# Performance work log

Measured on AMD Instinct MI355X. Metric: run time of the kernel, lower is better.

Reference implementation:

```python
import jax, jax.numpy as jnp
import numpy as np

NUM_EMBEDDINGS = 1024
EMBEDDING_DIM = 256

def setup_inputs() -> dict:
    key = jax.random.key(0)
    k1, k2 = jax.random.split(key)
    x = jax.random.normal(k1, (8, 16, 32, 32, EMBEDDING_DIM), dtype=jnp.float32)
    embeddings = jax.random.normal(k2, (NUM_EMBEDDINGS, EMBEDDING_DIM), dtype=jnp.float32)
    return {"x": x, "embeddings": embeddings}

def reference(x, embeddings):
    # Flatten all leading dims to tokens: [N, D]
    flat = x.reshape(-1, EMBEDDING_DIM)
    # Squared euclidean distances via ||a||^2 + ||b||^2 - 2 a.b  -> [N, K]
    sim = jnp.matmul(flat, embeddings.T)
    distances = (jnp.sum(flat * flat, axis=1, keepdims=True)
                 + jnp.sum(embeddings * embeddings, axis=1)
                 - 2.0 * sim)
    encoding_indices = jnp.argmin(distances, axis=1)  # [N]
    quantized = embeddings[encoding_indices].reshape(x.shape)
    # Perplexity from code usage histogram (mean of one-hot == normalized counts)
    counts = jnp.zeros((NUM_EMBEDDINGS,), dtype=jnp.float32).at[encoding_indices].add(1.0)
    avg_probs = counts / flat.shape[0]
    perplexity = jnp.exp(-jnp.sum(avg_probs * jnp.log(avg_probs + 1e-10)))
    return quantized, perplexity
```

## Files before the change

### kernel.cpp

```cpp
#include <hip/hip_runtime.h>
#include <math.h>
#include <stdint.h>

#define NTOK 131072
#define DIM  256
#define KEMB 1024

typedef _Float16 f16x8 __attribute__((ext_vector_type(8)));
typedef float    f32x4 __attribute__((ext_vector_type(4)));

#define FLAG_CAP 65536
#define FLAG_THR 8u

static __device__ __forceinline__ unsigned umin32(unsigned a, unsigned b){ return a<b?a:b; }
static __device__ __forceinline__ unsigned umax32(unsigned a, unsigned b){ return a>b?a:b; }

static __device__ __forceinline__ void gload_lds16(const void* g, void* l) {
    __builtin_amdgcn_global_load_lds(
        (const __attribute__((address_space(1))) unsigned int*)g,
        (__attribute__((address_space(3))) unsigned int*)l, 16, 0, 0);
}

static __device__ __forceinline__ void split_hl(const float4& f0, const float4& f1,
                                                f16x8& h, f16x8& l) {
    float v[8] = {f0.x, f0.y, f0.z, f0.w, f1.x, f1.y, f1.z, f1.w};
    #pragma unroll
    for (int e = 0; e < 8; ++e) {
        const _Float16 hi = (_Float16)v[e];
        h[e] = hi;
        l[e] = (_Float16)(v[e] - (float)hi);
    }
}

__global__ __launch_bounds__(64) void prep_kernel(const float* __restrict__ emb,
                                                  float* __restrict__ eNorm,
                                                  float* __restrict__ cst2,
                                                  unsigned* __restrict__ counts,
                                                  unsigned* __restrict__ flagCnt,
                                                  _Float16* __restrict__ img_hi,
                                                  _Float16* __restrict__ img_lo,
                                                  _Float16* __restrict__ img2) {
    const int k = blockIdx.x;
    const int lane = threadIdx.x;
    const float4 v = *reinterpret_cast<const float4*>(emb + (size_t)k * DIM + lane * 4);
    float s = v.x * v.x + v.y * v.y + v.z * v.z + v.w * v.w;
    #pragma unroll
    for (int m = 32; m; m >>= 1) s += __shfl_xor(s, m, 64);
    if (lane == 0) {
        eNorm[k] = s;
        cst2[k]  = s + 512.0f;
        counts[k] = 0u;
        if (k == 0) *flagCnt = 0u;
    }
    if (lane < 32) {
        const int p = lane;
        const int sl = p ^ (k & 7);
        const float4 s0 = *reinterpret_cast<const float4*>(emb + (size_t)k * DIM + sl * 8);
        const float4 s1 = *reinterpret_cast<const float4*>(emb + (size_t)k * DIM + sl * 8 + 4);
        f16x8 h, l;
        split_hl(s0, s1, h, l);
        *reinterpret_cast<f16x8*>(img_hi + (size_t)k * 256 + p * 8) = h;
        *reinterpret_cast<f16x8*>(img_lo + (size_t)k * 256 + p * 8) = l;
        const int kk = p >> 2, g = p & 3;
        const int ec = k >> 4, c = k & 15;
        const float4 f0 = *reinterpret_cast<const float4*>(emb + (size_t)k * DIM + p * 8);
        const float4 f1 = *reinterpret_cast<const float4*>(emb + (size_t)k * DIM + p * 8 + 4);
        f16x8 h2, l2;
        split_hl(f0, f1, h2, l2);
        *reinterpret_cast<f16x8*>(img2 + (size_t)ec * 4096 + kk * 512 + (g * 16 + c) * 8) = h2;
    }
}

__global__ __launch_bounds__(256, 2) void vq_main(const float* __restrict__ x,
                                                  const float* __restrict__ emb,
                                                  const _Float16* __restrict__ img2,
                                                  const float* __restrict__ cst2,
                                                  int* __restrict__ idxArr,
                                                  unsigned* __restrict__ counts,
                                                  unsigned* __restrict__ flagCnt,
                                                  unsigned* __restrict__ flagList,
                                                  float* __restrict__ out) {
    __shared__ int idx_s[256];

    const int tid  = threadIdx.x;
    const int wv   = tid >> 6;
    const int lane = tid & 63;
    const int g    = lane >> 4;
    const int c    = lane & 15;
    const int T0   = blockIdx.x * 256;
    const int T0w  = T0 + wv * 64;

    f16x8 a[4][8];
    #pragma unroll
    for (int i = 0; i < 4; ++i) {
        const float* xr = x + (size_t)(T0w + i * 16 + c) * DIM + g * 8;
        #pragma unroll
        for (int kk = 0; kk < 8; ++kk) {
            const float4 f0 = *reinterpret_cast<const float4*>(xr + kk * 32);
            const float4 f1 = *reinterpret_cast<const float4*>(xr + kk * 32 + 4);
            a[i][kk] = (f16x8){(_Float16)f0.x, (_Float16)f0.y, (_Float16)f0.z, (_Float16)f0.w,
                               (_Float16)f1.x, (_Float16)f1.y, (_Float16)f1.z, (_Float16)f1.w};
        }
    }

    unsigned m1[16], m2[16];
    #pragma unroll
    for (int t = 0; t < 16; ++t) { m1[t] = 0xFFFFFFFFu; m2[t] = 0xFFFFFFFFu; }

    const _Float16* ibase = img2 + lane * 8;

#define LOADB(DST, CSTD, EC) do {                                              \
        _Pragma("unroll")                                                      \
        for (int _kk = 0; _kk < 8; ++_kk)                                      \
            DST[_kk] = *reinterpret_cast<const f16x8*>(                        \
                ibase + (size_t)(EC) * 4096 + _kk * 512);                      \
        CSTD = cst2[(EC) * 16 + c];                                            \
    } while (0)

#define COMPUTE(BUF, CST, EC) do {                                             \
        f32x4 _acc[4];                                                         \
        _Pragma("unroll")                                                      \
        for (int _i = 0; _i < 4; ++_i) _acc[_i] = (f32x4){0.f, 0.f, 0.f, 0.f}; \
        _Pragma("unroll")                                                      \
        for (int _kk = 0; _kk < 8; ++_kk)                                      \
            _Pragma("unroll")                                                  \
            for (int _i = 0; _i < 4; ++_i)                                     \
                _acc[_i] = __builtin_amdgcn_mfma_f32_16x16x32_f16(             \
                    a[_i][_kk], BUF[_kk], _acc[_i], 0, 0, 0);                  \
        const int _col = (EC) * 16 + c;                                        \
        _Pragma("unroll")                                                      \
        for (int _i = 0; _i < 4; ++_i)                                         \
            _Pragma("unroll")                                                  \
            for (int _e = 0; _e < 4; ++_e) {                                   \
                const float    _d = fmaf(_acc[_i][_e], -2.0f, CST);            \
                const unsigned _k = (__builtin_bit_cast(unsigned, _d)          \
                                     & 0xFFFFFC00u) | (unsigned)_col;          \
                const int _t = _i * 4 + _e;                                    \
                m2[_t] = umin32(m2[_t], umax32(_k, m1[_t]));                   \
                m1[_t] = umin32(m1[_t], _k);                                   \
            }                                                                  \
    } while (0)

    f16x8 bA[8], bB[8];
    float cstA, cstB;
    LOADB(bA, cstA, 0);

    for (int ec2 = 0; ec2 < 32; ++ec2) {
        const int ec0 = ec2 * 2;
        LOADB(bB, cstB, ec0 + 1);
        COMPUTE(bA, cstA, ec0);
        if (ec0 + 2 < 64) LOADB(bA, cstA, ec0 + 2);
        COMPUTE(bB, cstB, ec0 + 1);
    }
#undef LOADB
#undef COMPUTE

    #pragma unroll
    for (int off = 1; off < 16; off <<= 1) {
        #pragma unroll
        for (int t = 0; t < 16; ++t) {
            const unsigned o1 = __shfl_xor(m1[t], off, 64);
            const unsigned o2 = __shfl_xor(m2[t], off, 64);
            const unsigned nm2 = umin32(umin32(m2[t], o2), umax32(m1[t], o1));
            m1[t] = umin32(m1[t], o1);
            m2[t] = nm2;
        }
    }

    if (c == 0) {
        #pragma unroll
        for (int t = 0; t < 16; ++t) {
            const int i   = t >> 2;
            const int e   = t & 3;
            const int row = i * 16 + g * 4 + e;
            const int idx = (int)(m1[t] & 1023u);
            idx_s[wv * 64 + row] = idx;
            idxArr[T0w + row] = idx;
            atomicAdd(&counts[idx], 1u);
            if (((m2[t] >> 10) - (m1[t] >> 10)) < FLAG_THR) {
                const unsigned pos = atomicAdd(flagCnt, 1u);
                if (pos < FLAG_CAP) flagList[pos] = (unsigned)(T0w + row);
            }
        }
    }
    __syncthreads();

    #pragma unroll 4
    for (int s = 0; s < 64; ++s) {
        const int fi  = s * 256 + tid;
        const int row = fi >> 6;
        const int q4  = fi & 63;
        const int em  = idx_s[row];
        *reinterpret_cast<float4*>(out + (size_t)(T0 + row) * DIM + q4 * 4) =
            *reinterpret_cast<const float4*>(emb + (size_t)em * DIM + q4 * 4);
    }
}

__global__ __launch_bounds__(256) void fixup_refine(const float* __restrict__ x,
                                                    const _Float16* __restrict__ img_hi,
                                                    const _Float16* __restrict__ img_lo,
                                                    const float* __restrict__ cst2,
                                                    const unsigned* __restrict__ flagCnt,
                                                    const unsigned* __restrict__ flagList,
                                                    uint2* __restrict__ refTop) {
    __shared__ _Float16 Bh[16384];
    __shared__ _Float16 Bl[16384];
    __shared__ float cst_s[1024];

    const unsigned nf = umin32(*flagCnt, (unsigned)FLAG_CAP);
    if (blockIdx.x * 64u >= nf) return;

    const int tid  = threadIdx.x;
    const int wv   = tid >> 6;
    const int lane = tid & 63;
    const int g    = lane >> 4;
    const int c    = lane & 15;
    const unsigned base = (blockIdx.x * 4u + (unsigned)wv) * 16u;

    *reinterpret_cast<float4*>(&cst_s[tid * 4]) =
        *reinterpret_cast<const float4*>(&cst2[tid * 4]);

    const unsigned myTok = flagList[(base + c) < nf ? (base + c) : 0];
    f16x8 ah[8], al[8];
    {
        const float* xr = x + (size_t)myTok * DIM + g * 8;
        #pragma unroll
        for (int kk = 0; kk < 8; ++kk) {
            const float4 f0 = *reinterpret_cast<const float4*>(xr + kk * 32);
            const float4 f1 = *reinterpret_cast<const float4*>(xr + kk * 32 + 4);
            split_hl(f0, f1, ah[kk], al[kk]);
        }
    }

    unsigned m1[4], m2[4];
    #pragma unroll
    for (int e = 0; e < 4; ++e) { m1[e] = 0xFFFFFFFFu; m2[e] = 0xFFFFFFFFu; }

    for (int ec = 0; ec < 16; ++ec) {
        __syncthreads();
        #pragma unroll
        for (int i = 0; i < 8; ++i) {
            gload_lds16((const char*)img_hi + ec * 32768 + (i * 256 + tid) * 16,
                        (char*)&Bh[0] + i * 4096 + wv * 1024);
            gload_lds16((const char*)img_lo + ec * 32768 + (i * 256 + tid) * 16,
                        (char*)&Bl[0] + i * 4096 + wv * 1024);
        }
        __syncthreads();

        f32x4 acc[4];
        #pragma unroll
        for (int j = 0; j < 4; ++j) acc[j] = (f32x4){0.f, 0.f, 0.f, 0.f};

        #pragma unroll
        for (int kk = 0; kk < 8; ++kk) {
            #pragma unroll
            for (int j = 0; j < 4; ++j) {
                const int row = j * 16 + c;
                const int off = row * 256 + (((kk * 4 + g) ^ (row & 7)) << 3);
                const f16x8 bh = *reinterpret_cast<const f16x8*>(&Bh[off]);
                const f16x8 bl = *reinterpret_cast<const f16x8*>(&Bl[off]);
                acc[j] = __builtin_amdgcn_mfma_f32_16x16x32_f16(ah[kk], bh, acc[j], 0, 0, 0);
                acc[j] = __builtin_amdgcn_mfma_f32_16x16x32_f16(ah[kk], bl, acc[j], 0, 0, 0);
                acc[j] = __builtin_amdgcn_mfma_f32_16x16x32_f16(al[kk], bh, acc[j], 0, 0, 0);
            }
        }

        #pragma unroll
        for (int j = 0; j < 4; ++j) {
            const int   col = ec * 64 + j * 16 + c;
            const float cst = cst_s[col];
            #pragma unroll
            for (int e = 0; e < 4; ++e) {
                const float    d   = fmaf(acc[j][e], -2.0f, cst);
                const unsigned key = (__builtin_bit_cast(unsigned, d) & 0xFFFFFC00u) | (unsigned)col;
                m2[e] = umin32(m2[e], umax32(key, m1[e]));
                m1[e] = umin32(m1[e], key);
            }
        }
    }

    #pragma unroll
    for (int off = 1; off < 16; off <<= 1) {
        #pragma unroll
        for (int e = 0; e < 4; ++e) {
            const unsigned o1 = __shfl_xor(m1[e], off, 64);
            const unsigned o2 = __shfl_xor(m2[e], off, 64);
            const unsigned nm2 = umin32(umin32(m2[e], o2), umax32(m1[e], o1));
            m1[e] = umin32(m1[e], o1);
            m2[e] = nm2;
        }
    }

    if (c == 0) {
        #pragma unroll
        for (int e = 0; e < 4; ++e) {
            const unsigned pos = base + (unsigned)(g * 4 + e);
            if (pos < nf) refTop[pos] = make_uint2(m1[e], m2[e]);
        }
    }
}

__global__ __launch_bounds__(256) void fixup_exact(const float* __restrict__ x,
                                                   const float* __restrict__ emb,
                                                   const float* __restrict__ eNorm,
                                                   const unsigned* __restrict__ flagCnt,
                                                   const unsigned* __restrict__ flagList,
                                                   const uint2* __restrict__ refTop,
                                                   int* __restrict__ idxArr,
                                                   unsigned* __restrict__ counts,
                                                   float* __restrict__ out) {
    const unsigned nf = umin32(*flagCnt, (unsigned)FLAG_CAP);
    const int tid  = threadIdx.x;
    const int wv   = tid >> 6;
    const int lane = tid & 63;

    for (unsigned pos = blockIdx.x * 4u + (unsigned)wv; pos < nf; pos += gridDim.x * 4u) {
        const unsigned tok = flagList[pos];
        const uint2 tk = refTop[pos];
        const int e1 = (int)(tk.x & 1023u);
        const int e2 = (int)(tk.y & 1023u);

        const float4 xv = *reinterpret_cast<const float4*>(x   + (size_t)tok * DIM + lane * 4);
        const float4 v1 = *reinterpret_cast<const float4*>(emb + (size_t)e1  * DIM + lane * 4);
        const float4 v2 = *reinterpret_cast<const float4*>(emb + (size_t)e2  * DIM + lane * 4);
        float p1 = xv.x * v1.x + xv.y * v1.y + xv.z * v1.z + xv.w * v1.w;
        float p2 = xv.x * v2.x + xv.y * v2.y + xv.z * v2.z + xv.w * v2.w;
        #pragma unroll
        for (int off = 1; off < 64; off <<= 1) {
            p1 += __shfl_xor(p1, off, 64);
            p2 += __shfl_xor(p2, off, 64);
        }
        const float d1 = eNorm[e1] - 2.0f * p1;
        const float d2 = eNorm[e2] - 2.0f * p2;
        const bool pick2 = (d2 < d1) || (d2 == d1 && e2 < e1);
        const int  ni   = pick2 ? e2 : e1;
        const int  old  = idxArr[tok];
        if (ni != old) {
            if (lane == 0) {
                idxArr[tok] = ni;
                atomicSub(&counts[old], 1u);
                atomicAdd(&counts[ni], 1u);
            }
            const float4 nv = pick2 ? v2 : v1;
            *reinterpret_cast<float4*>(out + (size_t)tok * DIM + lane * 4) = nv;
        }
    }
}

__global__ __launch_bounds__(256) void perp_kernel(const unsigned* __restrict__ counts,
                                                   float* __restrict__ out_perp) {
    __shared__ float red[256];
    const int tid = threadIdx.x;
    float s = 0.0f;
    for (int i = tid; i < KEMB; i += 256) {
        const float p = (float)counts[i] / (float)NTOK;
        s += p * logf(p + 1e-10f);
    }
    red[tid] = s;
    __syncthreads();
    for (int off = 128; off; off >>= 1) {
        if (tid < off) red[tid] += red[tid + off];
        __syncthreads();
    }
    if (tid == 0) *out_perp = expf(-red[0]);
}

extern "C" void kernel_launch(void* const* d_in, const int* in_sizes, int n_in,
                              void* d_out, int out_size, void* d_ws, size_t ws_size,
                              hipStream_t stream) {
    (void)in_sizes; (void)n_in; (void)out_size; (void)ws_size;
    const float* x   = (const float*)d_in[0];
    const float* emb = (const float*)d_in[1];
    float* out = (float*)d_out;

    char* ws = (char*)d_ws;
    float*     eNorm    = (float*)(ws);
    float*     cst2     = (float*)(ws + 4096);
    unsigned*  counts   = (unsigned*)(ws + 8192);
    unsigned*  flagCnt  = (unsigned*)(ws + 12288);
    unsigned*  flagList = (unsigned*)(ws + 16384);
    int*       idxArr   = (int*)(ws + 278528);
    _Float16*  img_hi   = (_Float16*)(ws + 802816);
    _Float16*  img_lo   = (_Float16*)(ws + 1327104);
    uint2*     refTop   = (uint2*)(ws + 1851392);
    _Float16*  img2     = (_Float16*)(ws + 2363392);

    prep_kernel<<<KEMB, 64, 0, stream>>>(emb, eNorm, cst2, counts, flagCnt,
                                         img_hi, img_lo, img2);
    vq_main<<<NTOK / 256, 256, 0, stream>>>(x, emb, img2, cst2, idxArr, counts,
                                            flagCnt, flagList, out);
    fixup_refine<<<1024, 256, 0, stream>>>(x, img_hi, img_lo, cst2, flagCnt, flagList, refTop);
    fixup_exact<<<2048, 256, 0, stream>>>(x, emb, eNorm, flagCnt, flagList, refTop,
                                          idxArr, counts, out);
    perp_kernel<<<1, 256, 0, stream>>>(counts, out + (size_t)NTOK * DIM);
}
```

Baseline: 207.2 us.

## Software-pipeline MFMA and argmin fold across codebook chunks, stage norms in LDS

Splits the per-chunk work into an MFMA phase and a distance/argmin fold phase, then interleaves them so the fold of one chunk overlaps the MFMAs of the next. This aims to hide the VALU fold latency behind matrix-core work. Codebook norms are also staged once into shared memory, which replaces per-chunk global loads and adds a block barrier. It costs a second set of accumulator registers, which could raise register pressure under the two-waves launch bound.

```diff
diff --git a/kernel.cpp b/kernel.cpp
--- a/kernel.cpp
+++ b/kernel.cpp
@@ -80,6 +80,7 @@
                                                   unsigned* __restrict__ flagCnt,
                                                   unsigned* __restrict__ flagList,
                                                   float* __restrict__ out) {
+    __shared__ float cst_s[1024];
     __shared__ int idx_s[256];
 
     const int tid  = threadIdx.x;
@@ -90,6 +91,9 @@
     const int T0   = blockIdx.x * 256;
     const int T0w  = T0 + wv * 64;
 
+    *reinterpret_cast<float4*>(&cst_s[tid * 4]) =
+        *reinterpret_cast<const float4*>(&cst2[tid * 4]);
+
     f16x8 a[4][8];
     #pragma unroll
     for (int i = 0; i < 4; ++i) {
@@ -109,30 +113,34 @@
 
     const _Float16* ibase = img2 + lane * 8;
 
-#define LOADB(DST, CSTD, EC) do {                                              \
+    __syncthreads();
+
+#define LOADB(DST, EC) do {                                                    \
         _Pragma("unroll")                                                      \
         for (int _kk = 0; _kk < 8; ++_kk)                                      \
             DST[_kk] = *reinterpret_cast<const f16x8*>(                        \
                 ibase + (size_t)(EC) * 4096 + _kk * 512);                      \
-        CSTD = cst2[(EC) * 16 + c];                                            \
     } while (0)
 
-#define COMPUTE(BUF, CST, EC) do {                                             \
-        f32x4 _acc[4];                                                         \
+#define MFMA_INTO(ACC, BUF) do {                                               \
         _Pragma("unroll")                                                      \
-        for (int _i = 0; _i < 4; ++_i) _acc[_i] = (f32x4){0.f, 0.f, 0.f, 0.f}; \
+        for (int _i = 0; _i < 4; ++_i) ACC[_i] = (f32x4){0.f, 0.f, 0.f, 0.f};  \
         _Pragma("unroll")                                                      \
         for (int _kk = 0; _kk < 8; ++_kk)                                      \
             _Pragma("unroll")                                                  \
             for (int _i = 0; _i < 4; ++_i)                                     \
-                _acc[_i] = __builtin_amdgcn_mfma_f32_16x16x32_f16(             \
-                    a[_i][_kk], BUF[_kk], _acc[_i], 0, 0, 0);                  \
-        const int _col = (EC) * 16 + c;                                        \
+                ACC[_i] = __builtin_amdgcn_mfma_f32_16x16x32_f16(              \
+                    a[_i][_kk], BUF[_kk], ACC[_i], 0, 0, 0);                   \
+    } while (0)
+
+#define FOLD(ACC, EC) do {                                                     \
+        const int   _col = (EC) * 16 + c;                                      \
+        const float _cst = cst_s[_col];                                        \
         _Pragma("unroll")                                                      \
         for (int _i = 0; _i < 4; ++_i)                                         \
             _Pragma("unroll")                                                  \
             for (int _e = 0; _e < 4; ++_e) {                                   \
-                const float    _d = fmaf(_acc[_i][_e], -2.0f, CST);            \
+                const float    _d = fmaf(ACC[_i][_e], -2.0f, _cst);            \
                 const unsigned _k = (__builtin_bit_cast(unsigned, _d)          \
                                      & 0xFFFFFC00u) | (unsigned)_col;          \
                 const int _t = _i * 4 + _e;                                    \
@@ -142,18 +150,26 @@
     } while (0)
 
     f16x8 bA[8], bB[8];
-    float cstA, cstB;
-    LOADB(bA, cstA, 0);
-
-    for (int ec2 = 0; ec2 < 32; ++ec2) {
-        const int ec0 = ec2 * 2;
-        LOADB(bB, cstB, ec0 + 1);
-        COMPUTE(bA, cstA, ec0);
-        if (ec0 + 2 < 64) LOADB(bA, cstA, ec0 + 2);
-        COMPUTE(bB, cstB, ec0 + 1);
-    }
+    f32x4 accA[4], accB[4];
+
+    LOADB(bA, 0);
+    MFMA_INTO(accA, bA);
+    LOADB(bB, 1);
+
+    for (int k = 0; k < 31; ++k) {
+        MFMA_INTO(accB, bB);
+        LOADB(bA, 2 * k + 2);
+        FOLD(accA, 2 * k);
+        MFMA_INTO(accA, bA);
+        LOADB(bB, 2 * k + 3);
+        FOLD(accB, 2 * k + 1);
+    }
+    MFMA_INTO(accB, bB);
+    FOLD(accA, 62);
+    FOLD(accB, 63);
 #undef LOADB
-#undef COMPUTE
+#undef MFMA_INTO
+#undef FOLD
 
     #pragma unroll
     for (int off = 1; off < 16; off <<= 1) {
```

New measurement: 224.7 us. +8.5%, slower.
